# Kernel optimization log

Measured on AMD Instinct MI355X. Metric: run time of the kernel, lower is better.

The kernel has to match this reference:

```python
import jax, jax.numpy as jnp
import numpy as np

B, C, H, W = 4, 128, 64, 64


def setup_inputs() -> dict:
    key = jax.random.key(0)
    k1, k2 = jax.random.split(key)
    x = jax.random.normal(k1, (B, C, H, W), dtype=jnp.float32)
    # 1x1 conv kv_mapper: weight [C_out, C_in], bias [C_out]; C_out == C_in == C
    W_kv = jax.random.normal(k2, (C, C), dtype=jnp.float32) * (1.0 / np.sqrt(C))
    b_kv = jnp.zeros((C,), dtype=jnp.float32)
    return {"x": x, "W_kv": W_kv, "b_kv": b_kv}


def reference(x, W_kv, b_kv):
    b, c, h, w = x.shape
    # kv_mapper: 1x1 conv  -> v: [b, c, h, w]
    v = jnp.einsum('bchw,oc->bohw', x, W_kv) + b_kv[None, :, None, None]
    # rearrange 'b c h w -> b (h w) c'
    L = h * w
    values = v.reshape(b, c, L).transpose(0, 2, 1)    # keys == values
    queries = x.reshape(b, c, L).transpose(0, 2, 1)
    # scaled dot-product attention, full [b, L, L] scores
    scores = jnp.einsum('blc,btc->blt', queries, values) / jnp.sqrt(jnp.asarray(c, x.dtype))
    attn = jax.nn.softmax(scores, axis=-1)
    out = jnp.einsum('blt,btv->blv', attn, values)    # [b, L, c]
    # rearrange 'b (h w) c -> b c h w'
    return out.transpose(0, 2, 1).reshape(b, c, h, w)
```

## Files before the change

kernel.cpp:

```cpp
#include <hip/hip_runtime.h>

#define LQ 4096
#define CH 128
#define NB 4
#define QSCALE 0.12753139626233174f
#define MAXCH 8
#define TILE_HW 8192

#if defined(__has_builtin)
#if __has_builtin(__builtin_amdgcn_mfma_f32_16x16x16bf16_1k)
#define HAVE_MFMA16 1
#endif
#endif

typedef __attribute__((ext_vector_type(8))) unsigned short ushort8;
typedef __attribute__((ext_vector_type(4))) unsigned short ushort4v;
typedef __attribute__((ext_vector_type(4))) short short4v;
typedef __attribute__((ext_vector_type(8))) __bf16 bf16x8;
typedef __attribute__((ext_vector_type(4))) float f32x4;

__device__ inline unsigned short f2bf(float f) {
    unsigned int u = __builtin_bit_cast(unsigned int, f);
    u += 0x7fffu + ((u >> 16) & 1u);
    return (unsigned short)(u >> 16);
}
__device__ inline float bf2f(unsigned short h) {
    unsigned int u = (unsigned int)h << 16;
    return __builtin_bit_cast(float, u);
}
__device__ inline unsigned int bfpack2(float a, float b) {
    unsigned int ua = __builtin_bit_cast(unsigned int, a) + 0x8000u;
    unsigned int ub = __builtin_bit_cast(unsigned int, b) + 0x8000u;
    return (ua >> 16) | (ub & 0xffff0000u);
}
__device__ inline void gload_lds16(const unsigned short* g, unsigned short* l) {
    __builtin_amdgcn_global_load_lds(
        (const __attribute__((address_space(1))) unsigned int*)(g),
        (__attribute__((address_space(3))) unsigned int*)(l), 16, 0, 0);
}

__global__ __launch_bounds__(256) void prep_kernel(
    const float* __restrict__ x, const float* __restrict__ Wkv,
    const float* __restrict__ bkv,
    unsigned short* __restrict__ Vt2, unsigned short* __restrict__ Vc2)
{
    __shared__ __align__(16) unsigned short xs[64 * 136];
    __shared__ __align__(16) unsigned short vs[128 * 72];
    const int tid = threadIdx.x;
    const int lane = tid & 63;
    const int wave = tid >> 6;
    const int quad = lane >> 4, l16 = lane & 15;
    const int b = blockIdx.x & 3;
    const int T = blockIdx.x >> 2;
    const int l0 = T << 6;

    {
        const f32x4* xg4 = (const f32x4*)(x + (size_t)b * CH * LQ + l0);
        #pragma unroll
        for (int i = 0; i < 8; ++i) {
            int idx = i * 256 + tid;
            int c = idx >> 4, l4 = idx & 15;
            f32x4 v = xg4[c * (LQ / 4) + l4];
            #pragma unroll
            for (int m = 0; m < 4; ++m) xs[(l4 * 4 + m) * 136 + c] = f2bf(v[m]);
        }
    }
    __syncthreads();

    const int wo = wave * 32;
    f32x4 acc[2][4];
    #pragma unroll
    for (int ot = 0; ot < 2; ++ot)
        #pragma unroll
        for (int lt = 0; lt < 4; ++lt) acc[ot][lt] = f32x4{0.f, 0.f, 0.f, 0.f};

    #pragma unroll
    for (int kc = 0; kc < 4; ++kc) {
        bf16x8 af[2];
        #pragma unroll
        for (int ot = 0; ot < 2; ++ot) {
            const float* wrow = Wkv + (size_t)(wo + ot * 16 + l16) * CH + kc * 32 + quad * 8;
            f32x4 w0 = *(const f32x4*)(wrow);
            f32x4 w1 = *(const f32x4*)(wrow + 4);
            ushort8 a;
            #pragma unroll
            for (int j = 0; j < 4; ++j) { a[j] = f2bf(w0[j]); a[j + 4] = f2bf(w1[j]); }
            af[ot] = __builtin_bit_cast(bf16x8, a);
        }
        #pragma unroll
        for (int lt = 0; lt < 4; ++lt) {
            bf16x8 bf = __builtin_bit_cast(bf16x8,
                *(const ushort8*)(xs + (lt * 16 + l16) * 136 + kc * 32 + quad * 8));
            #pragma unroll
            for (int ot = 0; ot < 2; ++ot)
                acc[ot][lt] = __builtin_amdgcn_mfma_f32_16x16x32_bf16(af[ot], bf, acc[ot][lt], 0, 0, 0);
        }
    }
    #pragma unroll
    for (int ot = 0; ot < 2; ++ot) {
        float bias[4];
        #pragma unroll
        for (int r = 0; r < 4; ++r) bias[r] = bkv[wo + ot * 16 + quad * 4 + r];
        #pragma unroll
        for (int lt = 0; lt < 4; ++lt)
            #pragma unroll
            for (int r = 0; r < 4; ++r)
                vs[(wo + ot * 16 + quad * 4 + r) * 72 + lt * 16 + l16] =
                    f2bf(acc[ot][lt][r] + bias[r]);
    }
    __syncthreads();
    const size_t tbase = ((size_t)b * 64 + T) * TILE_HW;
    #pragma unroll
    for (int i = 0; i < 4; ++i) {
        const int ci = i * 256 + tid;
        const int g = ci >> 6, ls = ci & 63;
        const int nt = g >> 2, kc = g & 3, qs = ls >> 4, l16s = ls & 15;
        ushort8 v;
        #pragma unroll
        for (int j = 0; j < 8; ++j) v[j] = vs[(kc * 32 + qs * 8 + j) * 72 + nt * 16 + l16s];
        *(ushort8*)(Vt2 + tbase + (size_t)ci * 8) = v;
    }
    #pragma unroll
    for (int i = 0; i < 4; ++i) {
        const int ci = i * 256 + tid;
        const int g = ci >> 6, ls = ci & 63;
        const int nt = g >> 2, p = g & 3, qs = ls >> 4, l16s = ls & 15;
        ushort4v a = *(const ushort4v*)(vs + (p * 32 + l16s) * 72 + nt * 16 + qs * 4);
        ushort4v c2 = *(const ushort4v*)(vs + (p * 32 + 16 + l16s) * 72 + nt * 16 + qs * 4);
        ushort8 v;
        #pragma unroll
        for (int j = 0; j < 4; ++j) { v[j] = a[j]; v[j + 4] = c2[j]; }
        *(ushort8*)(Vc2 + tbase + (size_t)ci * 8) = v;
    }
}

__global__ __launch_bounds__(256, 3) void attn_kernel(
    const float* __restrict__ x, const unsigned short* __restrict__ Vt2,
    const unsigned short* __restrict__ Vc2,
    unsigned short* __restrict__ Opart, float* __restrict__ Lsum, int titers)
{
    __shared__ __align__(16) unsigned short bufA[TILE_HW];
    __shared__ __align__(16) unsigned short bufB[TILE_HW];
    const int tid = threadIdx.x;
    const int wave = tid >> 6, lane = tid & 63;
    const int quad = lane >> 4, l16 = lane & 15;
    const int b = blockIdx.x & 3;
    const int rest = blockIdx.x >> 2;
    const int qtile = rest & 31;
    const int chunk = rest >> 5;
    const int q0w = (qtile << 7) + (wave << 5);
    const int Tbase = chunk * titers;

    const unsigned short* vtb = Vt2 + (size_t)b * 64 * TILE_HW;
    const unsigned short* vcb = Vc2 + (size_t)b * 64 * TILE_HW;

    bf16x8 qf[2][4];
    #pragma unroll
    for (int mt = 0; mt < 2; ++mt)
        #pragma unroll
        for (int kc = 0; kc < 4; ++kc) {
            ushort8 v;
            #pragma unroll
            for (int j = 0; j < 8; ++j) {
                int c = kc * 32 + quad * 8 + j;
                v[j] = f2bf(x[((size_t)b * CH + c) * LQ + q0w + mt * 16 + l16] * QSCALE);
            }
            qf[mt][kc] = __builtin_bit_cast(bf16x8, v);
        }

    f32x4 oacc[2][8];
    #pragma unroll
    for (int mt = 0; mt < 2; ++mt)
        #pragma unroll
        for (int i = 0; i < 8; ++i) oacc[mt][i] = f32x4{0.f, 0.f, 0.f, 0.f};
    float lsum[2] = {0.f, 0.f};

    auto issueA = [&](int T) {
        const unsigned short* sa = vtb + (size_t)T * TILE_HW + lane * 8;
        #pragma unroll
        for (int g = 0; g < 4; ++g) {
            const int go = (wave * 4 + g) * 512;
            gload_lds16(sa + go, &bufA[go]);
        }
    };
    auto issueB = [&](int T) {
        const unsigned short* sb = vcb + (size_t)T * TILE_HW + lane * 8;
        #pragma unroll
        for (int g = 0; g < 4; ++g) {
            const int go = (wave * 4 + g) * 512;
            gload_lds16(sb + go, &bufB[go]);
        }
    };
    issueA(Tbase);

    for (int it = 0; it < titers; ++it) {
        asm volatile("s_waitcnt vmcnt(0)" ::: "memory");
        __builtin_amdgcn_s_barrier();
        issueB(Tbase + it);

#ifdef HAVE_MFMA16
        short4v pf[4][2];
#else
        bf16x8 pf[4][2];
#endif
        #pragma unroll
        for (int nt = 0; nt < 4; ++nt) {
            bf16x8 vA[4];
            #pragma unroll
            for (int kc = 0; kc < 4; ++kc)
                vA[kc] = __builtin_bit_cast(bf16x8,
                    *(const ushort8*)(bufA + (nt * 4 + kc) * 512 + lane * 8));
            f32x4 s[2];
            __builtin_amdgcn_s_setprio(1);
            #pragma unroll
            for (int mt = 0; mt < 2; ++mt) {
                s[mt] = f32x4{0.f, 0.f, 0.f, 0.f};
                #pragma unroll
                for (int kc = 0; kc < 4; ++kc)
                    s[mt] = __builtin_amdgcn_mfma_f32_16x16x32_bf16(vA[kc], qf[mt][kc], s[mt], 0, 0, 0);
            }
            __builtin_amdgcn_s_setprio(0);
            #pragma unroll
            for (int mt = 0; mt < 2; ++mt) {
                float p0 = __builtin_amdgcn_exp2f(s[mt][0]);
                float p1 = __builtin_amdgcn_exp2f(s[mt][1]);
                float p2 = __builtin_amdgcn_exp2f(s[mt][2]);
                float p3 = __builtin_amdgcn_exp2f(s[mt][3]);
                lsum[mt] += (p0 + p1) + (p2 + p3);
                unsigned int lo = bfpack2(p0, p1);
                unsigned int hi = bfpack2(p2, p3);
#ifdef HAVE_MFMA16
                ushort4v pk;
                pk[0] = (unsigned short)lo; pk[1] = (unsigned short)(lo >> 16);
                pk[2] = (unsigned short)hi; pk[3] = (unsigned short)(hi >> 16);
                pf[nt][mt] = __builtin_bit_cast(short4v, pk);
#else
                ushort8 pk;
                pk[0] = (unsigned short)lo; pk[1] = (unsigned short)(lo >> 16);
                pk[2] = (unsigned short)hi; pk[3] = (unsigned short)(hi >> 16);
                pk[4] = 0; pk[5] = 0; pk[6] = 0; pk[7] = 0;
                pf[nt][mt] = __builtin_bit_cast(bf16x8, pk);
#endif
            }
        }

        asm volatile("s_waitcnt vmcnt(0)" ::: "memory");
        __builtin_amdgcn_s_barrier();
        if (it + 1 < titers) issueA(Tbase + it + 1);

        __builtin_amdgcn_s_setprio(1);
        #pragma unroll
        for (int nt = 0; nt < 4; ++nt) {
            #pragma unroll
            for (int p = 0; p < 4; ++p) {
                ushort8 d8 = *(const ushort8*)(bufB + (nt * 4 + p) * 512 + lane * 8);
                #pragma unroll
                for (int h = 0; h < 2; ++h) {
                    ushort4v f;
                    #pragma unroll
                    for (int j = 0; j < 4; ++j) f[j] = d8[h * 4 + j];
#ifdef HAVE_MFMA16
                    short4v vB = __builtin_bit_cast(short4v, f);
                    #pragma unroll
                    for (int mt = 0; mt < 2; ++mt)
                        oacc[mt][p * 2 + h] = __builtin_amdgcn_mfma_f32_16x16x16bf16_1k(
                            pf[nt][mt], vB, oacc[mt][p * 2 + h], 0, 0, 0);
#else
                    ushort8 vb;
                    #pragma unroll
                    for (int j = 0; j < 4; ++j) { vb[j] = f[j]; vb[j + 4] = 0; }
                    bf16x8 vB = __builtin_bit_cast(bf16x8, vb);
                    #pragma unroll
                    for (int mt = 0; mt < 2; ++mt)
                        oacc[mt][p * 2 + h] = __builtin_amdgcn_mfma_f32_16x16x32_bf16(
                            pf[nt][mt], vB, oacc[mt][p * 2 + h], 0, 0, 0);
#endif
                }
            }
        }
        __builtin_amdgcn_s_setprio(0);
    }
    const size_t pbase = ((size_t)(chunk * NB + b) * LQ);
    #pragma unroll
    for (int mt = 0; mt < 2; ++mt) {
        float v = lsum[mt];
        v += __shfl_xor(v, 16);
        v += __shfl_xor(v, 32);
        if (lane < 16) Lsum[pbase + q0w + mt * 16 + lane] = v;
    }
    #pragma unroll
    for (int mt = 0; mt < 2; ++mt)
        #pragma unroll
        for (int r = 0; r < 4; ++r) {
            const int q = q0w + mt * 16 + quad * 4 + r;
            unsigned short* orow = Opart + (pbase + q) * CH + l16;
            #pragma unroll
            for (int nc = 0; nc < 8; ++nc) orow[nc * 16] = f2bf(oacc[mt][nc][r]);
        }
}

__global__ __launch_bounds__(256) void combine_kernel(
    const unsigned short* __restrict__ Opart, const float* __restrict__ Lsum,
    float* __restrict__ out, int nchunk)
{
    __shared__ __align__(16) float ls[32 * 132];
    __shared__ float linv[32];
    const int tid = threadIdx.x;
    const int b = blockIdx.x & 3;
    const int q0 = (blockIdx.x >> 2) << 5;

    if (tid < 32) {
        float s = 0.f;
        for (int ch = 0; ch < nchunk; ++ch) s += Lsum[(size_t)(ch * NB + b) * LQ + q0 + tid];
        linv[tid] = 1.0f / s;
    }
    __syncthreads();
    {
        const int c8 = (tid & 15) * 8, qg = tid >> 4;
        #pragma unroll
        for (int i = 0; i < 2; ++i) {
            const int q = qg * 2 + i;
            float s[8];
            #pragma unroll
            for (int k = 0; k < 8; ++k) s[k] = 0.f;
            for (int ch = 0; ch < nchunk; ++ch) {
                ushort8 p = *(const ushort8*)(Opart +
                    ((size_t)(ch * NB + b) * LQ + q0 + q) * CH + c8);
                #pragma unroll
                for (int k = 0; k < 8; ++k) s[k] += bf2f(p[k]);
            }
            const float li = linv[q];
            f32x4 o0, o1;
            #pragma unroll
            for (int k = 0; k < 4; ++k) { o0[k] = s[k] * li; o1[k] = s[k + 4] * li; }
            *(f32x4*)(ls + q * 132 + c8) = o0;
            *(f32x4*)(ls + q * 132 + c8 + 4) = o1;
        }
    }
    __syncthreads();
    {
        const int c = tid & 127, qh = tid >> 7;
        float* dst = out + ((size_t)b * CH + c) * LQ + q0 + qh * 16;
        #pragma unroll
        for (int i = 0; i < 4; ++i) {
            f32x4 o;
            #pragma unroll
            for (int r = 0; r < 4; ++r) o[r] = ls[(qh * 16 + i * 4 + r) * 132 + c];
            ((f32x4*)dst)[i] = o;
        }
    }
}

extern "C" void kernel_launch(void* const* d_in, const int* in_sizes, int n_in,
                              void* d_out, int out_size, void* d_ws, size_t ws_size,
                              hipStream_t stream) {
    const float* x   = (const float*)d_in[0];
    const float* Wkv = (const float*)d_in[1];
    const float* bkv = (const float*)d_in[2];
    float* out = (float*)d_out;

    const size_t vElems = (size_t)NB * LQ * CH;
    unsigned short* Vt2 = (unsigned short*)d_ws;
    unsigned short* Vc2 = Vt2 + vElems;
    float* Lsum = (float*)(Vc2 + vElems);
    unsigned short* Opart = (unsigned short*)(Lsum + (size_t)MAXCH * NB * LQ);

    int nchunk = 8;
    const size_t fixed = 2 * vElems * 2 + (size_t)MAXCH * NB * LQ * 4;
    while (nchunk > 1 && fixed + (size_t)nchunk * NB * LQ * CH * 2 > ws_size) nchunk >>= 1;
    const int titers = (LQ / 64) / nchunk;

    prep_kernel<<<dim3(256), dim3(256), 0, stream>>>(x, Wkv, bkv, Vt2, Vc2);
    attn_kernel<<<dim3(128 * nchunk), dim3(256), 0, stream>>>(x, Vt2, Vc2, Opart, Lsum, titers);
    combine_kernel<<<dim3(512), dim3(256), 0, stream>>>(Opart, Lsum, out, nchunk);
}
```

Baseline: 124.4 us.

## Switch PV product to K=32 MFMA with re-laid-out V tiles

Replaces the PV product's 16x16x16 bf16 MFMAs with 16x16x32 MFMAs. Two score sub-tiles of P are packed into one 8-wide operand, and the V copy layout is rewritten so each lane loads a matching 8-element fragment. This halves the number of PV MFMA instructions and drops the per-element shuffles used to split 8-wide loads. The loop is also split into two halves so the PV MFMAs on the first half can start before all scores are done. Occupancy is raised to 4 blocks per CU and the first prefetch is issued before Q is loaded, at the cost of more register pressure and a changed barrier and wait pattern.

```diff
diff --git a/kernel.cpp b/kernel.cpp
--- a/kernel.cpp
+++ b/kernel.cpp
@@ -7,15 +7,8 @@
 #define MAXCH 8
 #define TILE_HW 8192
 
-#if defined(__has_builtin)
-#if __has_builtin(__builtin_amdgcn_mfma_f32_16x16x16bf16_1k)
-#define HAVE_MFMA16 1
-#endif
-#endif
-
 typedef __attribute__((ext_vector_type(8))) unsigned short ushort8;
 typedef __attribute__((ext_vector_type(4))) unsigned short ushort4v;
-typedef __attribute__((ext_vector_type(4))) short short4v;
 typedef __attribute__((ext_vector_type(8))) __bf16 bf16x8;
 typedef __attribute__((ext_vector_type(4))) float f32x4;
 
@@ -124,17 +117,18 @@
     for (int i = 0; i < 4; ++i) {
         const int ci = i * 256 + tid;
         const int g = ci >> 6, ls = ci & 63;
-        const int nt = g >> 2, p = g & 3, qs = ls >> 4, l16s = ls & 15;
-        ushort4v a = *(const ushort4v*)(vs + (p * 32 + l16s) * 72 + nt * 16 + qs * 4);
-        ushort4v c2 = *(const ushort4v*)(vs + (p * 32 + 16 + l16s) * 72 + nt * 16 + qs * 4);
+        const int a = g >> 3, nc = g & 7, qs = ls >> 4, l16s = ls & 15;
+        const int base = (nc * 16 + l16s) * 72 + a * 32 + qs * 4;
+        ushort4v lo4 = *(const ushort4v*)(vs + base);
+        ushort4v hi4 = *(const ushort4v*)(vs + base + 16);
         ushort8 v;
         #pragma unroll
-        for (int j = 0; j < 4; ++j) { v[j] = a[j]; v[j + 4] = c2[j]; }
+        for (int j = 0; j < 4; ++j) { v[j] = lo4[j]; v[j + 4] = hi4[j]; }
         *(ushort8*)(Vc2 + tbase + (size_t)ci * 8) = v;
     }
 }
 
-__global__ __launch_bounds__(256, 3) void attn_kernel(
+__global__ __launch_bounds__(256, 4) void attn_kernel(
     const float* __restrict__ x, const unsigned short* __restrict__ Vt2,
     const unsigned short* __restrict__ Vc2,
     unsigned short* __restrict__ Opart, float* __restrict__ Lsum, int titers)
@@ -154,6 +148,24 @@
     const unsigned short* vtb = Vt2 + (size_t)b * 64 * TILE_HW;
     const unsigned short* vcb = Vc2 + (size_t)b * 64 * TILE_HW;
 
+    auto issueA = [&](int T) {
+        const unsigned short* sa = vtb + (size_t)T * TILE_HW + lane * 8;
+        #pragma unroll
+        for (int g = 0; g < 4; ++g) {
+            const int go = (wave * 4 + g) * 512;
+            gload_lds16(sa + go, &bufA[go]);
+        }
+    };
+    auto issueB = [&](int T) {
+        const unsigned short* sb = vcb + (size_t)T * TILE_HW + lane * 8;
+        #pragma unroll
+        for (int g = 0; g < 4; ++g) {
+            const int go = (wave * 4 + g) * 512;
+            gload_lds16(sb + go, &bufB[go]);
+        }
+    };
+    issueA(Tbase);
+
     bf16x8 qf[2][4];
     #pragma unroll
     for (int mt = 0; mt < 2; ++mt)
@@ -174,111 +186,71 @@
         #pragma unroll
         for (int i = 0; i < 8; ++i) oacc[mt][i] = f32x4{0.f, 0.f, 0.f, 0.f};
     float lsum[2] = {0.f, 0.f};
-
-    auto issueA = [&](int T) {
-        const unsigned short* sa = vtb + (size_t)T * TILE_HW + lane * 8;
-        #pragma unroll
-        for (int g = 0; g < 4; ++g) {
-            const int go = (wave * 4 + g) * 512;
-            gload_lds16(sa + go, &bufA[go]);
-        }
-    };
-    auto issueB = [&](int T) {
-        const unsigned short* sb = vcb + (size_t)T * TILE_HW + lane * 8;
-        #pragma unroll
-        for (int g = 0; g < 4; ++g) {
-            const int go = (wave * 4 + g) * 512;
-            gload_lds16(sb + go, &bufB[go]);
-        }
-    };
-    issueA(Tbase);
 
     for (int it = 0; it < titers; ++it) {
         asm volatile("s_waitcnt vmcnt(0)" ::: "memory");
         __builtin_amdgcn_s_barrier();
         issueB(Tbase + it);
 
-#ifdef HAVE_MFMA16
-        short4v pf[4][2];
-#else
-        bf16x8 pf[4][2];
-#endif
-        #pragma unroll
-        for (int nt = 0; nt < 4; ++nt) {
-            bf16x8 vA[4];
-            #pragma unroll
-            for (int kc = 0; kc < 4; ++kc)
-                vA[kc] = __builtin_bit_cast(bf16x8,
-                    *(const ushort8*)(bufA + (nt * 4 + kc) * 512 + lane * 8));
-            f32x4 s[2];
+        unsigned int pk[2][4];
+
+        #pragma unroll
+        for (int a = 0; a < 2; ++a) {
+            #pragma unroll
+            for (int h = 0; h < 2; ++h) {
+                const int nt = a * 2 + h;
+                f32x4 s0 = f32x4{0.f, 0.f, 0.f, 0.f};
+                f32x4 s1 = f32x4{0.f, 0.f, 0.f, 0.f};
+                __builtin_amdgcn_s_setprio(1);
+                #pragma unroll
+                for (int kc = 0; kc < 4; ++kc) {
+                    bf16x8 vA = __builtin_bit_cast(bf16x8,
+                        *(const ushort8*)(bufA + (nt * 4 + kc) * 512 + lane * 8));
+                    s0 = __builtin_amdgcn_mfma_f32_16x16x32_bf16(vA, qf[0][kc], s0, 0, 0, 0);
+                    s1 = __builtin_amdgcn_mfma_f32_16x16x32_bf16(vA, qf[1][kc], s1, 0, 0, 0);
+                }
+                __builtin_amdgcn_s_setprio(0);
+                {
+                    float p0 = __builtin_amdgcn_exp2f(s0[0]);
+                    float p1 = __builtin_amdgcn_exp2f(s0[1]);
+                    float p2 = __builtin_amdgcn_exp2f(s0[2]);
+                    float p3 = __builtin_amdgcn_exp2f(s0[3]);
+                    lsum[0] += (p0 + p1) + (p2 + p3);
+                    pk[0][h * 2 + 0] = bfpack2(p0, p1);
+                    pk[0][h * 2 + 1] = bfpack2(p2, p3);
+                }
+                {
+                    float p0 = __builtin_amdgcn_exp2f(s1[0]);
+                    float p1 = __builtin_amdgcn_exp2f(s1[1]);
+                    float p2 = __builtin_amdgcn_exp2f(s1[2]);
+                    float p3 = __builtin_amdgcn_exp2f(s1[3]);
+                    lsum[1] += (p0 + p1) + (p2 + p3);
+                    pk[1][h * 2 + 0] = bfpack2(p0, p1);
+                    pk[1][h * 2 + 1] = bfpack2(p2, p3);
+                }
+            }
+
+            if (a == 0) {
+                asm volatile("s_waitcnt vmcnt(0)" ::: "memory");
+                __builtin_amdgcn_s_barrier();
+            } else {
+                asm volatile("s_waitcnt lgkmcnt(0)" ::: "memory");
+                __builtin_amdgcn_s_barrier();
+                if (it + 1 < titers) issueA(Tbase + it + 1);
+            }
+
+            bf16x8 pa0 = __builtin_bit_cast(bf16x8, pk[0]);
+            bf16x8 pa1 = __builtin_bit_cast(bf16x8, pk[1]);
             __builtin_amdgcn_s_setprio(1);
             #pragma unroll
-            for (int mt = 0; mt < 2; ++mt) {
-                s[mt] = f32x4{0.f, 0.f, 0.f, 0.f};
-                #pragma unroll
-                for (int kc = 0; kc < 4; ++kc)
-                    s[mt] = __builtin_amdgcn_mfma_f32_16x16x32_bf16(vA[kc], qf[mt][kc], s[mt], 0, 0, 0);
+            for (int nc = 0; nc < 8; ++nc) {
+                bf16x8 vB = __builtin_bit_cast(bf16x8,
+                    *(const ushort8*)(bufB + (a * 8 + nc) * 512 + lane * 8));
+                oacc[0][nc] = __builtin_amdgcn_mfma_f32_16x16x32_bf16(pa0, vB, oacc[0][nc], 0, 0, 0);
+                oacc[1][nc] = __builtin_amdgcn_mfma_f32_16x16x32_bf16(pa1, vB, oacc[1][nc], 0, 0, 0);
             }
             __builtin_amdgcn_s_setprio(0);
-            #pragma unroll
-            for (int mt = 0; mt < 2; ++mt) {
-                float p0 = __builtin_amdgcn_exp2f(s[mt][0]);
-                float p1 = __builtin_amdgcn_exp2f(s[mt][1]);
-                float p2 = __builtin_amdgcn_exp2f(s[mt][2]);
-                float p3 = __builtin_amdgcn_exp2f(s[mt][3]);
-                lsum[mt] += (p0 + p1) + (p2 + p3);
-                unsigned int lo = bfpack2(p0, p1);
-                unsigned int hi = bfpack2(p2, p3);
-#ifdef HAVE_MFMA16
-                ushort4v pk;
-                pk[0] = (unsigned short)lo; pk[1] = (unsigned short)(lo >> 16);
-                pk[2] = (unsigned short)hi; pk[3] = (unsigned short)(hi >> 16);
-                pf[nt][mt] = __builtin_bit_cast(short4v, pk);
-#else
-                ushort8 pk;
-                pk[0] = (unsigned short)lo; pk[1] = (unsigned short)(lo >> 16);
-                pk[2] = (unsigned short)hi; pk[3] = (unsigned short)(hi >> 16);
-                pk[4] = 0; pk[5] = 0; pk[6] = 0; pk[7] = 0;
-                pf[nt][mt] = __builtin_bit_cast(bf16x8, pk);
-#endif
-            }
-        }
-
-        asm volatile("s_waitcnt vmcnt(0)" ::: "memory");
-        __builtin_amdgcn_s_barrier();
-        if (it + 1 < titers) issueA(Tbase + it + 1);
-
-        __builtin_amdgcn_s_setprio(1);
-        #pragma unroll
-        for (int nt = 0; nt < 4; ++nt) {
-            #pragma unroll
-            for (int p = 0; p < 4; ++p) {
-                ushort8 d8 = *(const ushort8*)(bufB + (nt * 4 + p) * 512 + lane * 8);
-                #pragma unroll
-                for (int h = 0; h < 2; ++h) {
-                    ushort4v f;
-                    #pragma unroll
-                    for (int j = 0; j < 4; ++j) f[j] = d8[h * 4 + j];
-#ifdef HAVE_MFMA16
-                    short4v vB = __builtin_bit_cast(short4v, f);
-                    #pragma unroll
-                    for (int mt = 0; mt < 2; ++mt)
-                        oacc[mt][p * 2 + h] = __builtin_amdgcn_mfma_f32_16x16x16bf16_1k(
-                            pf[nt][mt], vB, oacc[mt][p * 2 + h], 0, 0, 0);
-#else
-                    ushort8 vb;
-                    #pragma unroll
-                    for (int j = 0; j < 4; ++j) { vb[j] = f[j]; vb[j + 4] = 0; }
-                    bf16x8 vB = __builtin_bit_cast(bf16x8, vb);
-                    #pragma unroll
-                    for (int mt = 0; mt < 2; ++mt)
-                        oacc[mt][p * 2 + h] = __builtin_amdgcn_mfma_f32_16x16x32_bf16(
-                            pf[nt][mt], vB, oacc[mt][p * 2 + h], 0, 0, 0);
-#endif
-                }
-            }
-        }
-        __builtin_amdgcn_s_setprio(0);
+        }
     }
     const size_t pbase = ((size_t)(chunk * NB + b) * LQ);
     #pragma unroll
```

After: 243.4 us. +95.7%, slower.
